# Kernel tuning notes

Hardware: AMD Instinct MI355X
Metric: run time of the kernel (lower is better)

## Reference

```python
import jax, jax.numpy as jnp
import numpy as np

B, L, D, H, M = 2, 1024, 1024, 16, 64
DH = D // H  # depth per head


def setup_inputs() -> dict:
    key = jax.random.key(0)
    ks = jax.random.split(key, 7)
    s = 0.02
    return {
        "x": jax.random.normal(ks[0], (B, L, D), jnp.float32),
        "Wq": jax.random.normal(ks[1], (D, D), jnp.float32) * s,
        "Wk": jax.random.normal(ks[2], (D, D), jnp.float32) * s,
        "Wv": jax.random.normal(ks[3], (D, D), jnp.float32) * s,
        "Wo": jax.random.normal(ks[4], (D, D), jnp.float32) * s,
        "rel_k_table": jax.random.normal(ks[5], (2 * M + 1, DH), jnp.float32) * s,
        "rel_v_table": jax.random.normal(ks[6], (2 * M + 1, DH), jnp.float32) * s,
    }


def _rel_idx(length, max_rel):
    # Shaw-style clipped relative position indices: [L, L] in [0, 2*max_rel]
    r = jnp.arange(length)
    return jnp.clip(r[None, :] - r[:, None], -max_rel, max_rel) + max_rel


def _split_heads(t):
    # [B, L, D] -> [B, H, L, DH]
    return t.reshape(B, L, H, DH).transpose(0, 2, 1, 3)


def reference(x, Wq, Wk, Wv, Wo, rel_k_table, rel_v_table):
    q = _split_heads(x @ Wq) * (DH ** -0.5)  # T2T scales q by d_head^-0.5
    k = _split_heads(x @ Wk)
    v = _split_heads(x @ Wv)

    idx = _rel_idx(L, M)
    rel_k = rel_k_table[idx]  # [L, L, DH] gathered keys-relative embeddings
    rel_v = rel_v_table[idx]  # [L, L, DH]

    # _relative_attention_inner(q, k, rel_k, transpose=True)
    logits = jnp.einsum('bhid,bhjd->bhij', q, k) + jnp.einsum('bhid,ijd->bhij', q, rel_k)
    w = jax.nn.softmax(logits, axis=-1)  # [B, H, L, L]; dropout_rate=0 / inference

    # _relative_attention_inner(w, v, rel_v, transpose=False)
    o = jnp.einsum('bhij,bhjd->bhid', w, v) + jnp.einsum('bhij,ijd->bhid', w, rel_v)

    # combine heads then output transform
    o = o.transpose(0, 2, 1, 3).reshape(B, L, D)
    return o @ Wo
```

## Files before the change

kernel.cpp:

```cpp
#include <hip/hip_runtime.h>
#include <hip/hip_bf16.h>
#include <math.h>

#define B_ 2
#define L_ 1024
#define D_ 1024
#define H_ 16
#define DH_ 64
#define M_ 64
#define R_ 129
#define NLD ((size_t)B_ * L_ * D_)
#define DD  ((size_t)D_ * D_)
#define QSCALE 0.18033688011112042f

using bf16x8 = __attribute__((ext_vector_type(8))) short;
using f32x4  = __attribute__((ext_vector_type(4))) float;

__device__ __forceinline__ unsigned short f2bf(float f) {
    unsigned int x = __builtin_bit_cast(unsigned int, f);
    unsigned int r = x + 0x7fffu + ((x >> 16) & 1u);
    return (unsigned short)(r >> 16);
}
__device__ __forceinline__ float bf2f(unsigned short u) {
    unsigned int x = ((unsigned int)u) << 16;
    return __builtin_bit_cast(float, x);
}

__global__ __launch_bounds__(256)
void prep(const float* __restrict__ x,
          const float* __restrict__ W0, const float* __restrict__ W1,
          const float* __restrict__ W2, const float* __restrict__ W3,
          const float* __restrict__ relk, const float* __restrict__ relv,
          unsigned short* __restrict__ xb, unsigned short* __restrict__ Wt,
          unsigned short* __restrict__ relkb, unsigned short* __restrict__ relvT)
{
    __shared__ float tile[32][33];
    const int bid = blockIdx.x, t = threadIdx.x;
    if (bid < 2048) {
        const int i = bid * 256 + t;
        float4 v = ((const float4*)x)[i];
        short4 o = { (short)f2bf(v.x), (short)f2bf(v.y), (short)f2bf(v.z), (short)f2bf(v.w) };
        ((short4*)xb)[i] = o;
    } else if (bid < 6144) {
        const int wb = bid - 2048;
        const int z = wb >> 10, rem = wb & 1023;
        const float* W = z == 0 ? W0 : z == 1 ? W1 : z == 2 ? W2 : W3;
        unsigned short* T = Wt + (size_t)z * DD;
        const int k0 = (rem >> 5) * 32, n0 = (rem & 31) * 32;
        const int r = t >> 3, c = (t & 7) * 4;
        float4 v = *(const float4*)&W[(size_t)(k0 + r) * D_ + n0 + c];
        tile[r][c] = v.x; tile[r][c + 1] = v.y; tile[r][c + 2] = v.z; tile[r][c + 3] = v.w;
        __syncthreads();
        short4 o = { (short)f2bf(tile[c][r]),     (short)f2bf(tile[c + 1][r]),
                     (short)f2bf(tile[c + 2][r]), (short)f2bf(tile[c + 3][r]) };
        *(short4*)&T[(size_t)(n0 + r) * D_ + k0 + c] = o;
    } else {
        const int idx = (bid - 6144) * 256 + t;
        if (idx < 144 * 64) {
            const int r = idx >> 6, d = idx & 63;
            relkb[idx] = (r < R_) ? f2bf(relk[r * 64 + d]) : (unsigned short)0;
        }
        if (idx < 64 * 136) {
            const int d = idx / 136, r = idx - d * 136;
            relvT[idx] = (r < R_) ? f2bf(relv[r * 64 + d]) : (unsigned short)0;
        }
    }
}

__global__ __launch_bounds__(256)
void gemm128(const unsigned short* __restrict__ A, const unsigned short* __restrict__ Bt,
             unsigned short* __restrict__ Cb, float* __restrict__ Cf, float scale0)
{
    __shared__ unsigned short As[128][64];
    __shared__ unsigned short Bs[128][64];

    const int t = threadIdx.x, lane = t & 63, wid = t >> 6;
    const int fr = lane & 15, g = lane >> 4;
    const int m0 = blockIdx.y * 128;
    const int nglob = blockIdx.x * 128;
    const int mat = nglob >> 10;
    const int n0 = nglob & 1023;
    const float scale = (mat == 0) ? scale0 : 1.f;
    const int wm = (wid >> 1) * 64, wn = (wid & 1) * 64;

    f32x4 acc[4][4] = {};

    int srow[4], skof[4], sdst[4];
#pragma unroll
    for (int c = 0; c < 4; ++c) {
        const int chunk = c * 256 + t;
        srow[c] = chunk >> 3;
        skof[c] = ((chunk & 7) ^ (srow[c] & 7)) * 8;
        sdst[c] = chunk * 8;
    }

    const unsigned short* Abase = A  + (size_t)m0 * D_;
    const unsigned short* Bbase = Bt + (size_t)nglob * D_;

    for (int k0 = 0; k0 < D_; k0 += 64) {
        __syncthreads();
#pragma unroll
        for (int c = 0; c < 4; ++c) {
            __builtin_amdgcn_global_load_lds(
                (const __attribute__((address_space(1))) void*)(Abase + (size_t)srow[c] * D_ + k0 + skof[c]),
                (__attribute__((address_space(3))) void*)(&As[0][0] + sdst[c]), 16, 0, 0);
            __builtin_amdgcn_global_load_lds(
                (const __attribute__((address_space(1))) void*)(Bbase + (size_t)srow[c] * D_ + k0 + skof[c]),
                (__attribute__((address_space(3))) void*)(&Bs[0][0] + sdst[c]), 16, 0, 0);
        }
        __syncthreads();

#pragma unroll
        for (int kb = 0; kb < 2; ++kb) {
            bf16x8 av[4], bv[4];
#pragma unroll
            for (int i = 0; i < 4; ++i) {
                const int ra = wm + i * 16 + fr;
                av[i] = *(const bf16x8*)&As[ra][(((kb << 2) + g) ^ (ra & 7)) * 8];
                const int rb = wn + i * 16 + fr;
                bv[i] = *(const bf16x8*)&Bs[rb][(((kb << 2) + g) ^ (rb & 7)) * 8];
            }
#pragma unroll
            for (int i = 0; i < 4; ++i)
#pragma unroll
                for (int j = 0; j < 4; ++j)
                    acc[i][j] = __builtin_amdgcn_mfma_f32_16x16x32_bf16(av[i], bv[j], acc[i][j], 0, 0, 0);
        }
    }

    const int orow = g * 4;
    if (Cb) {
        unsigned short* Cp = Cb + (size_t)mat * NLD;
#pragma unroll
        for (int i = 0; i < 4; ++i)
#pragma unroll
            for (int j = 0; j < 4; ++j) {
                unsigned short* cp = Cp + (size_t)(m0 + wm + i * 16 + orow) * D_ + n0 + wn + j * 16 + fr;
#pragma unroll
                for (int rg = 0; rg < 4; ++rg)
                    cp[(size_t)rg * D_] = f2bf(acc[i][j][rg] * scale);
            }
    } else {
#pragma unroll
        for (int i = 0; i < 4; ++i)
#pragma unroll
            for (int j = 0; j < 4; ++j) {
                float* cp = Cf + (size_t)(m0 + wm + i * 16 + orow) * D_ + n0 + wn + j * 16 + fr;
#pragma unroll
                for (int rg = 0; rg < 4; ++rg)
                    cp[(size_t)rg * D_] = acc[i][j][rg] * scale;
            }
    }
}

__device__ __forceinline__ void stage_k(const unsigned short* src, unsigned short* dst, int t)
{
#pragma unroll
    for (int it = 0; it < 2; ++it) {
        const int c = it * 256 + t;
        const int j = c >> 3;
        const int sc = (c & 7) ^ (j & 7);
        __builtin_amdgcn_global_load_lds(
            (const __attribute__((address_space(1))) void*)(src + (size_t)j * D_ + sc * 8),
            (__attribute__((address_space(3))) void*)(dst + c * 8), 16, 0, 0);
    }
}

__device__ __forceinline__ void write_vt(unsigned short (*Vtl)[64], int jp, int d0, bf16x8 a, bf16x8 b)
{
    const int jlo = (2 * jp) & 7;
    const int jc  = jp >> 2;
#pragma unroll
    for (int e = 0; e < 8; ++e) {
        const int d = d0 + e;
        const unsigned int val = (unsigned int)(unsigned short)a[e]
                               | ((unsigned int)(unsigned short)b[e] << 16);
        *(unsigned int*)&Vtl[d][((jc ^ (d & 7)) << 3) + jlo] = val;
    }
}

__global__ __launch_bounds__(256)
void attn_mfma(const unsigned short* __restrict__ Qb, const unsigned short* __restrict__ Kb,
               const unsigned short* __restrict__ Vb,
               const unsigned short* __restrict__ relkb,
               const unsigned short* __restrict__ relvT,
               const float* __restrict__ relv,
               unsigned short* __restrict__ Ob)
{
    __shared__ unsigned short Klds[2][64][64];
    __shared__ unsigned short Vt[2][64][64];
    __shared__ unsigned short Plds[64][72];
    __shared__ unsigned short QRs[64][128];
    __shared__ unsigned short Wsum[64][136];

    const int t    = threadIdx.x;
    const int lane = t & 63;
    const int w    = t >> 6;
    const int fr   = lane & 15;
    const int g    = lane >> 4;
    const int rg0  = g * 4;

    const int bx  = blockIdx.x;
    const int xcd = bx & 7, slot = bx >> 3;
    const int bh  = (xcd << 2) | (slot >> 4);
    const int rb  = slot & 15;
    const int b   = bh >> 4, h = bh & 15;
    const int i0  = rb * 64;
    const size_t head = (size_t)b * L_ * D_ + (size_t)h * DH_;

    const unsigned short* Kh = Kb + head;
    const unsigned short* Vh = Vb + head;

    stage_k(Kh, &Klds[0][0][0], t);

    const int jp = t & 31, d0v = ((t >> 5) & 7) * 8;
    bf16x8 va  = *(const bf16x8*)(Vh + (size_t)(2 * jp) * D_ + d0v);
    bf16x8 vb2 = *(const bf16x8*)(Vh + (size_t)(2 * jp + 1) * D_ + d0v);

    {
        unsigned int* wp = (unsigned int*)&Wsum[0][0];
        for (int i = t; i < 64 * 136 / 2; i += 256) wp[i] = 0u;
    }

    bf16x8 qf[2];
    {
        const unsigned short* qp = Qb + head + (size_t)(i0 + w * 16 + fr) * D_;
        qf[0] = *(const bf16x8*)(qp + g * 8);
        qf[1] = *(const bf16x8*)(qp + 32 + g * 8);
    }

    float qr0[4], qr128[4];
#pragma unroll
    for (int rc = 0; rc < 9; ++rc) {
        f32x4 acc = {};
#pragma unroll
        for (int kb = 0; kb < 2; ++kb) {
            bf16x8 rv = *(const bf16x8*)&relkb[(size_t)(rc * 16 + fr) * 64 + kb * 32 + g * 8];
            acc = __builtin_amdgcn_mfma_f32_16x16x32_bf16(qf[kb], rv, acc, 0, 0, 0);
        }
        if (rc < 8) {
#pragma unroll
            for (int reg = 0; reg < 4; ++reg)
                QRs[w * 16 + rg0 + reg][rc * 16 + fr] = f2bf(acc[reg]);
        }
        if (rc == 0) {
#pragma unroll
            for (int reg = 0; reg < 4; ++reg) qr0[reg] = __shfl(acc[reg], g * 16, 64);
        }
        if (rc == 8) {
#pragma unroll
            for (int reg = 0; reg < 4; ++reg) qr128[reg] = __shfl(acc[reg], g * 16, 64);
        }
    }

    write_vt(Vt[0], jp, d0v, va, vb2);
    asm volatile("s_waitcnt vmcnt(0)" ::: "memory");
    __syncthreads();

    f32x4 oacc[4] = {};
    float lpart[4] = {}, pe0p[4] = {}, pe128p[4] = {};

    int bb = 0;
    for (int jt = 0; jt < 16; ++jt) {
        const bool pre = (jt < 15);
        if (pre) {
            stage_k(Kh + (size_t)(jt + 1) * 64 * D_, &Klds[bb ^ 1][0][0], t);
            const unsigned short* vp = Vh + (size_t)((jt + 1) * 64 + 2 * jp) * D_ + d0v;
            va  = *(const bf16x8*)vp;
            vb2 = *(const bf16x8*)(vp + D_);
        }

        f32x4 s[4];
#pragma unroll
        for (int fc = 0; fc < 4; ++fc) {
            f32x4 a = {};
            const int j = fc * 16 + fr;
#pragma unroll
            for (int kb = 0; kb < 2; ++kb) {
                bf16x8 kv = *(const bf16x8*)&Klds[bb][j][(((kb << 2) + g) ^ (j & 7)) * 8];
                a = __builtin_amdgcn_mfma_f32_16x16x32_bf16(qf[kb], kv, a, 0, 0, 0);
            }
            s[fc] = a;
        }

        const int dt = (jt - rb) * 64;
        if (dt <= -128 || dt >= 128) {
            const bool lo = dt < 0;
#pragma unroll
            for (int reg = 0; reg < 4; ++reg) {
                const float qrc = lo ? qr0[reg] : qr128[reg];
                float rsum = 0.f;
#pragma unroll
                for (int fc = 0; fc < 4; ++fc) {
                    float pe = exp2f(s[fc][reg] + qrc);
                    rsum += pe;
                    Plds[w * 16 + rg0 + reg][fc * 16 + fr] = f2bf(pe);
                }
                lpart[reg] += rsum;
                if (lo) pe0p[reg] += rsum; else pe128p[reg] += rsum;
            }
        } else {
#pragma unroll
            for (int fc = 0; fc < 4; ++fc) {
#pragma unroll
                for (int reg = 0; reg < 4; ++reg) {
                    const int li  = w * 16 + rg0 + reg;
                    const int rel = dt + fc * 16 + fr - li;
                    float bias;
                    if (rel <= -M_)     bias = qr0[reg];
                    else if (rel >= M_) bias = qr128[reg];
                    else                bias = bf2f(QRs[li][rel + M_]);
                    float pe = exp2f(s[fc][reg] + bias);
                    lpart[reg] += pe;
                    Plds[li][fc * 16 + fr] = f2bf(pe);
                    if (rel <= -M_)      pe0p[reg]   += pe;
                    else if (rel >= M_)  pe128p[reg] += pe;
                    else                 Wsum[li][rel + M_] = f2bf(pe);
                }
            }
        }

        asm volatile("s_waitcnt lgkmcnt(0)" ::: "memory");

        bf16x8 pa0 = *(const bf16x8*)&Plds[w * 16 + fr][g * 8];
        bf16x8 pa1 = *(const bf16x8*)&Plds[w * 16 + fr][32 + g * 8];
#pragma unroll
        for (int fd = 0; fd < 4; ++fd) {
            const int d = fd * 16 + fr;
            bf16x8 vv0 = *(const bf16x8*)&Vt[bb][d][((g)     ^ (d & 7)) * 8];
            bf16x8 vv1 = *(const bf16x8*)&Vt[bb][d][((4 + g) ^ (d & 7)) * 8];
            oacc[fd] = __builtin_amdgcn_mfma_f32_16x16x32_bf16(pa0, vv0, oacc[fd], 0, 0, 0);
            oacc[fd] = __builtin_amdgcn_mfma_f32_16x16x32_bf16(pa1, vv1, oacc[fd], 0, 0, 0);
        }

        if (pre) write_vt(Vt[bb ^ 1], jp, d0v, va, vb2);
        asm volatile("s_waitcnt vmcnt(0)" ::: "memory");
        __syncthreads();
        bb ^= 1;
    }

#pragma unroll
    for (int m = 1; m <= 8; m <<= 1) {
#pragma unroll
        for (int reg = 0; reg < 4; ++reg) {
            lpart[reg]  += __shfl_xor(lpart[reg],  m, 64);
            pe0p[reg]   += __shfl_xor(pe0p[reg],   m, 64);
            pe128p[reg] += __shfl_xor(pe128p[reg], m, 64);
        }
    }
    if (fr == 0) {
#pragma unroll
        for (int reg = 0; reg < 4; ++reg) {
            Wsum[w * 16 + rg0 + reg][0]   = f2bf(pe0p[reg]);
            Wsum[w * 16 + rg0 + reg][128] = f2bf(pe128p[reg]);
        }
    }
    asm volatile("s_waitcnt lgkmcnt(0)" ::: "memory");
    __syncthreads();

#pragma unroll
    for (int kc = 0; kc < 4; ++kc) {
        bf16x8 wa = *(const bf16x8*)&Wsum[w * 16 + fr][kc * 32 + g * 8];
#pragma unroll
        for (int fd = 0; fd < 4; ++fd) {
            bf16x8 rv = *(const bf16x8*)&relvT[(size_t)(fd * 16 + fr) * 136 + kc * 32 + g * 8];
            oacc[fd] = __builtin_amdgcn_mfma_f32_16x16x32_bf16(wa, rv, oacc[fd], 0, 0, 0);
        }
    }

    float inv[4];
#pragma unroll
    for (int reg = 0; reg < 4; ++reg) inv[reg] = 1.f / lpart[reg];

#pragma unroll
    for (int fd = 0; fd < 4; ++fd) {
        const float r128 = relv[128 * 64 + fd * 16 + fr];
        unsigned short* op = Ob + head + (size_t)(i0 + w * 16 + rg0) * D_ + fd * 16 + fr;
#pragma unroll
        for (int reg = 0; reg < 4; ++reg)
            op[(size_t)reg * D_] = f2bf((oacc[fd][reg] + pe128p[reg] * r128) * inv[reg]);
    }
}

extern "C" void kernel_launch(void* const* d_in, const int* in_sizes, int n_in,
                              void* d_out, int out_size, void* d_ws, size_t ws_size,
                              hipStream_t stream)
{
    const float* x    = (const float*)d_in[0];
    const float* Wq   = (const float*)d_in[1];
    const float* Wk   = (const float*)d_in[2];
    const float* Wv   = (const float*)d_in[3];
    const float* Wo   = (const float*)d_in[4];
    const float* relk = (const float*)d_in[5];
    const float* relv = (const float*)d_in[6];
    float* out = (float*)d_out;

    unsigned short* xb    = (unsigned short*)d_ws;
    unsigned short* Wt    = xb + NLD;
    unsigned short* relkb = Wt + 4 * DD;
    unsigned short* relvT = relkb + 144 * 64;
    unsigned short* QKVb  = relvT + 64 * 136;
    unsigned short* Ob    = QKVb + 3 * NLD;

    prep<<<dim3(6180), 256, 0, stream>>>(x, Wq, Wk, Wv, Wo, relk, relv, xb, Wt, relkb, relvT);

    gemm128<<<dim3(24, 16), 256, 0, stream>>>(xb, Wt, QKVb, nullptr, QSCALE);

    attn_mfma<<<dim3(512), 256, 0, stream>>>(QKVb, QKVb + NLD, QKVb + 2 * NLD,
                                             relkb, relvT, relv, Ob);

    gemm128<<<dim3(8, 16), 256, 0, stream>>>(Ob, Wt + 3 * DD, nullptr, out, 1.f);
}
```

Measured before the change: 94.71 us.

## Transpose QK MFMA operands so each lane owns one query row

Swaps the MFMA operand order for the QK^T and Q·relk products so each lane holds four consecutive key columns of a single query row. Row sums then need only two cross-group shuffles instead of a 16-lane butterfly, and P and QR values can be packed and written to LDS as 64-bit stores. The relative-bias lookup becomes a clamped column index, with a dedicated diagonal-tile path. The change also adds s_setprio around the MFMA blocks and replaces the final barrier with a sched_barrier, which relies on each wave reading only its own Wsum rows.

```diff
diff --git a/kernel.cpp b/kernel.cpp
--- a/kernel.cpp
+++ b/kernel.cpp
@@ -24,6 +24,9 @@
 __device__ __forceinline__ float bf2f(unsigned short u) {
     unsigned int x = ((unsigned int)u) << 16;
     return __builtin_bit_cast(float, x);
+}
+__device__ __forceinline__ unsigned int pk2bf(float lo, float hi) {
+    return (unsigned int)f2bf(lo) | ((unsigned int)f2bf(hi) << 16);
 }
 
 __global__ __launch_bounds__(256)
@@ -190,7 +193,7 @@
     __shared__ unsigned short Klds[2][64][64];
     __shared__ unsigned short Vt[2][64][64];
     __shared__ unsigned short Plds[64][72];
-    __shared__ unsigned short QRs[64][128];
+    __shared__ unsigned short QRs[64][136];
     __shared__ unsigned short Wsum[64][136];
 
     const int t    = threadIdx.x;
@@ -198,7 +201,6 @@
     const int w    = t >> 6;
     const int fr   = lane & 15;
     const int g    = lane >> 4;
-    const int rg0  = g * 4;
 
     const int bx  = blockIdx.x;
     const int xcd = bx & 7, slot = bx >> 3;
@@ -208,6 +210,8 @@
     const int i0  = rb * 64;
     const size_t head = (size_t)b * L_ * D_ + (size_t)h * DH_;
 
+    const int iloc = w * 16 + fr;
+
     const unsigned short* Kh = Kb + head;
     const unsigned short* Vh = Vb + head;
 
@@ -224,32 +228,24 @@
 
     bf16x8 qf[2];
     {
-        const unsigned short* qp = Qb + head + (size_t)(i0 + w * 16 + fr) * D_;
+        const unsigned short* qp = Qb + head + (size_t)(i0 + iloc) * D_;
         qf[0] = *(const bf16x8*)(qp + g * 8);
         qf[1] = *(const bf16x8*)(qp + 32 + g * 8);
     }
 
-    float qr0[4], qr128[4];
 #pragma unroll
     for (int rc = 0; rc < 9; ++rc) {
         f32x4 acc = {};
 #pragma unroll
         for (int kb = 0; kb < 2; ++kb) {
             bf16x8 rv = *(const bf16x8*)&relkb[(size_t)(rc * 16 + fr) * 64 + kb * 32 + g * 8];
-            acc = __builtin_amdgcn_mfma_f32_16x16x32_bf16(qf[kb], rv, acc, 0, 0, 0);
+            acc = __builtin_amdgcn_mfma_f32_16x16x32_bf16(rv, qf[kb], acc, 0, 0, 0);
         }
         if (rc < 8) {
-#pragma unroll
-            for (int reg = 0; reg < 4; ++reg)
-                QRs[w * 16 + rg0 + reg][rc * 16 + fr] = f2bf(acc[reg]);
-        }
-        if (rc == 0) {
-#pragma unroll
-            for (int reg = 0; reg < 4; ++reg) qr0[reg] = __shfl(acc[reg], g * 16, 64);
-        }
-        if (rc == 8) {
-#pragma unroll
-            for (int reg = 0; reg < 4; ++reg) qr128[reg] = __shfl(acc[reg], g * 16, 64);
+            uint2 pk = { pk2bf(acc[0], acc[1]), pk2bf(acc[2], acc[3]) };
+            *(uint2*)&QRs[iloc][rc * 16 + g * 4] = pk;
+        } else if (g == 0) {
+            QRs[iloc][128] = f2bf(acc[0]);
         }
     }
 
@@ -257,8 +253,11 @@
     asm volatile("s_waitcnt vmcnt(0)" ::: "memory");
     __syncthreads();
 
+    const float qr0   = bf2f(QRs[iloc][0]);
+    const float qr128 = bf2f(QRs[iloc][128]);
+
     f32x4 oacc[4] = {};
-    float lpart[4] = {}, pe0p[4] = {}, pe128p[4] = {};
+    float lpart = 0.f, pe0p = 0.f, pe128p = 0.f;
 
     int bb = 0;
     for (int jt = 0; jt < 16; ++jt) {
@@ -271,6 +270,7 @@
         }
 
         f32x4 s[4];
+        __builtin_amdgcn_s_setprio(1);
 #pragma unroll
         for (int fc = 0; fc < 4; ++fc) {
             f32x4 a = {};
@@ -278,52 +278,72 @@
 #pragma unroll
             for (int kb = 0; kb < 2; ++kb) {
                 bf16x8 kv = *(const bf16x8*)&Klds[bb][j][(((kb << 2) + g) ^ (j & 7)) * 8];
-                a = __builtin_amdgcn_mfma_f32_16x16x32_bf16(qf[kb], kv, a, 0, 0, 0);
+                a = __builtin_amdgcn_mfma_f32_16x16x32_bf16(kv, qf[kb], a, 0, 0, 0);
             }
             s[fc] = a;
         }
-
-        const int dt = (jt - rb) * 64;
+        __builtin_amdgcn_s_setprio(0);
+
+        const int dt   = (jt - rb) * 64;
+        const int relb = dt - iloc + g * 4;
+
         if (dt <= -128 || dt >= 128) {
-            const bool lo = dt < 0;
-#pragma unroll
-            for (int reg = 0; reg < 4; ++reg) {
-                const float qrc = lo ? qr0[reg] : qr128[reg];
-                float rsum = 0.f;
-#pragma unroll
-                for (int fc = 0; fc < 4; ++fc) {
-                    float pe = exp2f(s[fc][reg] + qrc);
-                    rsum += pe;
-                    Plds[w * 16 + rg0 + reg][fc * 16 + fr] = f2bf(pe);
+            const float qrc = (dt < 0) ? qr0 : qr128;
+            float tsum = 0.f;
+#pragma unroll
+            for (int fc = 0; fc < 4; ++fc) {
+                float p0 = exp2f(s[fc][0] + qrc);
+                float p1 = exp2f(s[fc][1] + qrc);
+                float p2 = exp2f(s[fc][2] + qrc);
+                float p3 = exp2f(s[fc][3] + qrc);
+                uint2 pk = { pk2bf(p0, p1), pk2bf(p2, p3) };
+                *(uint2*)&Plds[iloc][fc * 16 + g * 4] = pk;
+                tsum += (p0 + p1) + (p2 + p3);
+            }
+            lpart += tsum;
+            if (dt < 0) pe0p += tsum; else pe128p += tsum;
+        } else if (dt == 0) {
+#pragma unroll
+            for (int fc = 0; fc < 4; ++fc) {
+                const int c0 = relb + fc * 16 + M_;
+                float pe[4];
+#pragma unroll
+                for (int reg = 0; reg < 4; ++reg) {
+                    pe[reg] = exp2f(s[fc][reg] + bf2f(QRs[iloc][c0 + reg]));
+                    lpart += pe[reg];
                 }
-                lpart[reg] += rsum;
-                if (lo) pe0p[reg] += rsum; else pe128p[reg] += rsum;
+                uint2 pk = { pk2bf(pe[0], pe[1]), pk2bf(pe[2], pe[3]) };
+                *(uint2*)&Plds[iloc][fc * 16 + g * 4] = pk;
+                Wsum[iloc][c0 + 0] = (unsigned short)(pk.x & 0xffffu);
+                Wsum[iloc][c0 + 1] = (unsigned short)(pk.x >> 16);
+                Wsum[iloc][c0 + 2] = (unsigned short)(pk.y & 0xffffu);
+                Wsum[iloc][c0 + 3] = (unsigned short)(pk.y >> 16);
             }
         } else {
 #pragma unroll
             for (int fc = 0; fc < 4; ++fc) {
+                float pe[4];
 #pragma unroll
                 for (int reg = 0; reg < 4; ++reg) {
-                    const int li  = w * 16 + rg0 + reg;
-                    const int rel = dt + fc * 16 + fr - li;
-                    float bias;
-                    if (rel <= -M_)     bias = qr0[reg];
-                    else if (rel >= M_) bias = qr128[reg];
-                    else                bias = bf2f(QRs[li][rel + M_]);
-                    float pe = exp2f(s[fc][reg] + bias);
-                    lpart[reg] += pe;
-                    Plds[li][fc * 16 + fr] = f2bf(pe);
-                    if (rel <= -M_)      pe0p[reg]   += pe;
-                    else if (rel >= M_)  pe128p[reg] += pe;
-                    else                 Wsum[li][rel + M_] = f2bf(pe);
+                    const int colr = relb + fc * 16 + reg + M_;
+                    const int col  = colr < 0 ? 0 : (colr > 128 ? 128 : colr);
+                    pe[reg] = exp2f(s[fc][reg] + bf2f(QRs[iloc][col]));
+                    lpart += pe[reg];
+                    if (col == 0)        pe0p   += pe[reg];
+                    else if (col == 128) pe128p += pe[reg];
+                    else                 Wsum[iloc][col] = f2bf(pe[reg]);
                 }
+                uint2 pk = { pk2bf(pe[0], pe[1]), pk2bf(pe[2], pe[3]) };
+                *(uint2*)&Plds[iloc][fc * 16 + g * 4] = pk;
             }
         }
 
         asm volatile("s_waitcnt lgkmcnt(0)" ::: "memory");
-
-        bf16x8 pa0 = *(const bf16x8*)&Plds[w * 16 + fr][g * 8];
-        bf16x8 pa1 = *(const bf16x8*)&Plds[w * 16 + fr][32 + g * 8];
+        __builtin_amdgcn_sched_barrier(0);
+
+        bf16x8 pa0 = *(const bf16x8*)&Plds[iloc][g * 8];
+        bf16x8 pa1 = *(const bf16x8*)&Plds[iloc][32 + g * 8];
+        __builtin_amdgcn_s_setprio(1);
 #pragma unroll
         for (int fd = 0; fd < 4; ++fd) {
             const int d = fd * 16 + fr;
@@ -332,6 +352,7 @@
             oacc[fd] = __builtin_amdgcn_mfma_f32_16x16x32_bf16(pa0, vv0, oacc[fd], 0, 0, 0);
             oacc[fd] = __builtin_amdgcn_mfma_f32_16x16x32_bf16(pa1, vv1, oacc[fd], 0, 0, 0);
         }
+        __builtin_amdgcn_s_setprio(0);
 
         if (pre) write_vt(Vt[bb ^ 1], jp, d0v, va, vb2);
         asm volatile("s_waitcnt vmcnt(0)" ::: "memory");
@@ -339,28 +360,19 @@
         bb ^= 1;
     }
 
-#pragma unroll
-    for (int m = 1; m <= 8; m <<= 1) {
-#pragma unroll
-        for (int reg = 0; reg < 4; ++reg) {
-            lpart[reg]  += __shfl_xor(lpart[reg],  m, 64);
-            pe0p[reg]   += __shfl_xor(pe0p[reg],   m, 64);
-            pe128p[reg] += __shfl_xor(pe128p[reg], m, 64);
-        }
-    }
-    if (fr == 0) {
-#pragma unroll
-        for (int reg = 0; reg < 4; ++reg) {
-            Wsum[w * 16 + rg0 + reg][0]   = f2bf(pe0p[reg]);
-            Wsum[w * 16 + rg0 + reg][128] = f2bf(pe128p[reg]);
-        }
+    lpart  += __shfl_xor(lpart, 16);  lpart  += __shfl_xor(lpart, 32);
+    pe0p   += __shfl_xor(pe0p, 16);   pe0p   += __shfl_xor(pe0p, 32);
+    pe128p += __shfl_xor(pe128p, 16); pe128p += __shfl_xor(pe128p, 32);
+    if (g == 0) {
+        Wsum[iloc][0]   = f2bf(pe0p);
+        Wsum[iloc][128] = f2bf(pe128p);
     }
     asm volatile("s_waitcnt lgkmcnt(0)" ::: "memory");
-    __syncthreads();
+    __builtin_amdgcn_sched_barrier(0);
 
 #pragma unroll
     for (int kc = 0; kc < 4; ++kc) {
-        bf16x8 wa = *(const bf16x8*)&Wsum[w * 16 + fr][kc * 32 + g * 8];
+        bf16x8 wa = *(const bf16x8*)&Wsum[iloc][kc * 32 + g * 8];
 #pragma unroll
         for (int fd = 0; fd < 4; ++fd) {
             bf16x8 rv = *(const bf16x8*)&relvT[(size_t)(fd * 16 + fr) * 136 + kc * 32 + g * 8];
@@ -368,17 +380,21 @@
         }
     }
 
-    float inv[4];
-#pragma unroll
-    for (int reg = 0; reg < 4; ++reg) inv[reg] = 1.f / lpart[reg];
+    float invd[4], pr128[4];
+#pragma unroll
+    for (int reg = 0; reg < 4; ++reg) {
+        const int src = (lane & 48) | (g * 4 + reg);
+        invd[reg]  = 1.f / __shfl(lpart, src, 64);
+        pr128[reg] = __shfl(pe128p, src, 64);
+    }
 
 #pragma unroll
     for (int fd = 0; fd < 4; ++fd) {
         const float r128 = relv[128 * 64 + fd * 16 + fr];
-        unsigned short* op = Ob + head + (size_t)(i0 + w * 16 + rg0) * D_ + fd * 16 + fr;
+        unsigned short* op = Ob + head + (size_t)(i0 + w * 16 + g * 4) * D_ + fd * 16 + fr;
 #pragma unroll
         for (int reg = 0; reg < 4; ++reg)
-            op[(size_t)reg * D_] = f2bf((oacc[fd][reg] + pe128p[reg] * r128) * inv[reg]);
+            op[(size_t)reg * D_] = f2bf((oacc[fd][reg] + pr128[reg] * r128) * invd[reg]);
     }
 }
 
```

Result: faster. 91.63 us (-3.2%).
